# Optimization experiments

Measured on AMD Instinct MI355X. Metric: run time of the kernel, lower is better.

## Reference

```python
import jax, jax.numpy as jnp
from jax import lax
import numpy as np

B = 2048
NUM_COMPO = 650
NUM_CHARS = 27533
COMPO_SCORE_THRESH = 0.7
SCORE_ADJ_SCALE = 0.1
K = 10  # top-k chars and max padded hit indices


def setup_inputs() -> dict:
    key = jax.random.key(0)
    k1, k2, k3, k4, k5 = jax.random.split(key, 5)
    return {
        "pred_class_logits": jax.random.normal(k1, (B, NUM_CHARS), dtype=jnp.float32),
        "pred_compo_logits": jax.random.normal(k2, (B, NUM_COMPO), dtype=jnp.float32),
        "chinese_char_ids": jax.random.randint(k3, (B,), 0, NUM_CHARS, dtype=jnp.int32),
        "compo_co_occurrence_prob": jax.random.uniform(k4, (NUM_COMPO, NUM_COMPO), dtype=jnp.float32),
        "compo_chinese_matrix": jax.random.randint(k5, (NUM_COMPO, NUM_CHARS), 0, 2, dtype=jnp.int32),
    }


def _components_to_char(compo_scores, co_occ, matrix):
    """Per-sample: compo_scores [C], co_occ [C,C], matrix [C,V] (0/1 int)."""
    # score adjustment: sum over compos with score>0.88 of co_occ row * score * scale
    hi = compo_scores > 0.88
    w = jnp.where(hi, compo_scores, 0.0)                       # [C]
    adjusted = compo_scores + SCORE_ADJ_SCALE * (w @ co_occ)   # [C]
    max_idx = jnp.argmax(adjusted)
    max_score = compo_scores[max_idx]

    # select compos above threshold, sorted descending by score
    sel = compo_scores > COMPO_SCORE_THRESH
    num_sel = jnp.sum(sel.astype(jnp.int32))
    masked = jnp.where(sel, compo_scores, -jnp.inf)
    order = jnp.argsort(-masked)                                # selected first, desc
    sorted_scores = jnp.take(compo_scores, order)               # [C]

    hit0 = matrix[max_idx]                                      # [V] int

    def cond(st):
        i, hit, _prev = st
        return (i < num_sel) & (jnp.sum(hit) > 1)

    def body(st):
        i, hit, _prev = st
        comp = matrix[order[i]]
        new_hit = ((hit + comp) == 2).astype(hit.dtype)         # intersection
        return (i + 1, new_hit, hit)

    i, hit, prev = lax.while_loop(cond, body, (jnp.int32(1), hit0, hit0))
    num_hit = jnp.sum(hit)
    empty = num_hit == 0
    i = jnp.where(empty, i - 1, i)
    hit = jnp.where(empty, prev, hit)
    hit_score = jnp.where(i == 1, max_score, sorted_scores[i - 1])

    # first K indices where hit == 1, padded with -1 (fixed shape)
    ar = jnp.arange(NUM_CHARS, dtype=jnp.int32)
    vals = jnp.where(hit == 1, NUM_CHARS - ar, 0)
    topv, topi = lax.top_k(vals, K)
    hit_indices = jnp.where(topv > 0, topi.astype(jnp.int32), -1)
    return adjusted, hit_indices, hit_score


def reference(pred_class_logits, pred_compo_logits, chinese_char_ids,
              compo_co_occurrence_prob, compo_chinese_matrix):
    class_probs = jax.nn.softmax(pred_class_logits, axis=1)     # [B, V]
    compo_scores = jax.nn.sigmoid(pred_compo_logits)            # [B, C]
    class_scores, class_indices = lax.top_k(class_probs, K)     # [B, K]

    adjusted, hit_idx, hit_scores = jax.vmap(
        _components_to_char, in_axes=(0, None, None)
    )(compo_scores, compo_co_occurrence_prob, compo_chinese_matrix)

    num_hit = jnp.sum((hit_idx != -1).astype(jnp.int32), axis=1)  # [B]
    pred1 = jnp.where(num_hit == 1, hit_idx[:, 0], class_indices[:, 0])
    pred2 = jnp.where((class_scores[:, 0] < 0.85) & (num_hit == 1),
                      hit_idx[:, 0], class_indices[:, 0])

    hit_compare = jnp.any(class_indices[:, :, None] == hit_idx[:, None, :], axis=2)  # [B,K]
    j = jnp.argmax(hit_compare, axis=1)  # first True (all-False -> 0), matches stable desc argsort[0]
    pred3 = class_indices[jnp.arange(class_indices.shape[0]), j]

    return (class_indices, class_scores, compo_scores, adjusted,
            hit_idx, hit_scores, pred1, pred2, pred3)
```

## Files before the change

kernel.cpp:

```cpp
#include <hip/hip_runtime.h>
#include <math.h>

#define NB 2048
#define NC 650
#define NV 27533
#define NK 10
#define NWRD 861
#define NT 256
#define NCHUNK 11
#define CHPR 431

__global__ __launch_bounds__(NT) void pack_kernel(const int* __restrict__ mat,
                                                  unsigned* __restrict__ packed) {
  const int lane = threadIdx.x & 63;
  const int wave = (blockIdx.x * NT + threadIdx.x) >> 6;
  const int nw = (gridDim.x * NT) >> 6;
  for (int t = wave; t < NC * CHPR; t += nw) {
    int c = t / CHPR;
    int ch = t - c * CHPR;
    int e = (ch << 6) + lane;
    int val = (e < NV) ? mat[(size_t)c * NV + e] : 0;
    unsigned long long m = __ballot(val != 0);
    if (lane == 0) {
      size_t base = (size_t)c * NWRD + (ch << 1);
      packed[base] = (unsigned)m;
      if ((ch << 1) + 1 < NWRD) packed[base + 1] = (unsigned)(m >> 32);
    }
  }
}

__device__ __forceinline__ int block_sum(int v, volatile int* red4, int tid) {
#pragma unroll
  for (int off = 32; off > 0; off >>= 1) v += __shfl_down(v, off);
  if ((tid & 63) == 0) red4[tid >> 6] = v;
  __syncthreads();
  int tot = red4[0] + red4[1] + red4[2] + red4[3];
  __syncthreads();
  return tot;
}

__global__ __launch_bounds__(NT, 6) void gen_pred_kernel(
    const float* __restrict__ class_logits,
    const float* __restrict__ compo_logits,
    const float* __restrict__ co_occ,
    const unsigned* __restrict__ packed,
    float* __restrict__ out) {
  const int b = blockIdx.x;
  const int tid = threadIdx.x;
  const int lane = tid & 63;
  const int wid = tid >> 6;

  __shared__ __align__(16) char arena[10464];
  float* mv = (float*)arena;
  int* mi = (int*)(arena + 5120);
  float* s_score = (float*)arena;
  int* s_selidx = (int*)(arena + 2608);
  int* s_hi = (int*)(arena + 5216);
  int* s_order = (int*)(arena + 7824);

  __shared__ float red_f[4];
  __shared__ int red_i[4];
  __shared__ int s_cls_idx[NK];
  __shared__ float s_cls_sc[NK];
  __shared__ int s_hit[NK];
  __shared__ int s_hicnt[NCHUNK];
  __shared__ int s_selcnt[NCHUNK];

  const size_t o_cidx = 0;
  const size_t o_csc = (size_t)NB * NK;
  const size_t o_comp = 2 * (size_t)NB * NK;
  const size_t o_adj = o_comp + (size_t)NB * NC;
  const size_t o_hidx = o_adj + (size_t)NB * NC;
  const size_t o_hsc = o_hidx + (size_t)NB * NK;
  const size_t o_p1 = o_hsc + NB;
  const size_t o_p2 = o_p1 + NB;
  const size_t o_p3 = o_p2 + NB;

  const float* lg = class_logits + (size_t)b * NV;
  float tv[NK];
  int ti[NK];
#pragma unroll
  for (int k = 0; k < NK; k++) { tv[k] = -INFINITY; ti[k] = 0x7fffffff; }
  float ssum = 0.f;

#define PROC(val, idxv)                                                   \
  {                                                                       \
    float v_ = (val);                                                     \
    ssum += __expf(v_);                                                   \
    if (v_ > tv[NK - 1]) {                                                \
      tv[NK - 1] = v_; ti[NK - 1] = (idxv);                               \
      _Pragma("unroll")                                                   \
      for (int p_ = NK - 1; p_ > 0; p_--) {                               \
        if (tv[p_] > tv[p_ - 1]) {                                        \
          float t0_ = tv[p_]; tv[p_] = tv[p_ - 1]; tv[p_ - 1] = t0_;      \
          int t1_ = ti[p_]; ti[p_] = ti[p_ - 1]; ti[p_ - 1] = t1_;        \
        }                                                                 \
      }                                                                   \
    }                                                                     \
  }

  const int s0 = (4 - (b & 3)) & 3;
  const int M4 = (NV - s0) >> 2;
  if (tid < s0) PROC(lg[tid], tid);
  {
    const float4* lg4 = (const float4*)(lg + s0);
    int v = tid;
    float4 f;
    if (v < M4) f = lg4[v];
    while (v < M4) {
      int vn = v + NT;
      float4 fn = f;
      if (vn < M4) fn = lg4[vn];
      int base = s0 + (v << 2);
      PROC(f.x, base);
      PROC(f.y, base + 1);
      PROC(f.z, base + 2);
      PROC(f.w, base + 3);
      f = fn;
      v = vn;
    }
  }
  {
    int baseT = s0 + (M4 << 2);
    if (tid < NV - baseT) PROC(lg[baseT + tid], baseT + tid);
  }
#undef PROC

  {
    float s = ssum;
#pragma unroll
    for (int off = 32; off > 0; off >>= 1) s += __shfl_down(s, off);
    if (lane == 0) red_f[wid] = s;
  }
  __syncthreads();
  const float Sv = red_f[0] + red_f[1] + red_f[2] + red_f[3];
  __syncthreads();

  if (tid >= 128) {
#pragma unroll
    for (int k = 0; k < NK; k++) {
      mv[(tid - 128) * NK + k] = tv[k];
      mi[(tid - 128) * NK + k] = ti[k];
    }
  }
  __syncthreads();
  if (tid < 128) {
    float rv[NK]; int ri[NK];
    int pa = 0, pb = 0;
    int bb = tid * NK;
#pragma unroll
    for (int k = 0; k < NK; k++) {
      float va = tv[pa]; int ia = ti[pa];
      float vb = mv[bb + pb]; int ib = mi[bb + pb];
      bool ta = (va > vb) || (va == vb && ia < ib);
      if (ta) { rv[k] = va; ri[k] = ia; pa++; }
      else { rv[k] = vb; ri[k] = ib; pb++; }
    }
#pragma unroll
    for (int k = 0; k < NK; k++) { mv[bb + k] = rv[k]; mi[bb + k] = ri[k]; }
  }
  __syncthreads();
  for (int st = 64; st > 0; st >>= 1) {
    if (tid < st) {
      float rv[NK]; int ri[NK];
      int pa = 0, pb = 0;
      int ba = tid * NK, bb = (tid + st) * NK;
#pragma unroll
      for (int k = 0; k < NK; k++) {
        float va = mv[ba + pa]; int ia = mi[ba + pa];
        float vb = mv[bb + pb]; int ib = mi[bb + pb];
        bool ta = (va > vb) || (va == vb && ia < ib);
        if (ta) { rv[k] = va; ri[k] = ia; pa++; }
        else { rv[k] = vb; ri[k] = ib; pb++; }
      }
#pragma unroll
      for (int k = 0; k < NK; k++) { mv[ba + k] = rv[k]; mi[ba + k] = ri[k]; }
    }
    __syncthreads();
  }
  if (tid < NK) {
    int cidx = mi[tid];
    float sc = __expf(mv[tid]) / Sv;
    s_cls_idx[tid] = cidx;
    s_cls_sc[tid] = sc;
    out[o_cidx + (size_t)b * NK + tid] = (float)cidx;
    out[o_csc + (size_t)b * NK + tid] = sc;
  }
  __syncthreads();

  const float* cl = compo_logits + (size_t)b * NC;
  for (int j = tid; j < NC; j += NT) {
    float x = cl[j];
    float sc = 1.f / (1.f + expf(-x));
    s_score[j] = sc;
    out[o_comp + (size_t)b * NC + j] = sc;
  }
  __syncthreads();

  for (int c = wid; c < NCHUNK; c += 4) {
    int e = (c << 6) + lane;
    float s = (e < NC) ? s_score[e] : 0.f;
    unsigned long long mh = __ballot(s > 0.88f);
    unsigned long long ms = __ballot(s > 0.7f);
    if (lane == 0) { s_hicnt[c] = __popcll(mh); s_selcnt[c] = __popcll(ms); }
  }
  __syncthreads();
  int nhi = 0, nsel = 0;
#pragma unroll
  for (int q = 0; q < NCHUNK; q++) { nhi += s_hicnt[q]; nsel += s_selcnt[q]; }
  for (int c = wid; c < NCHUNK; c += 4) {
    int e = (c << 6) + lane;
    float s = (e < NC) ? s_score[e] : 0.f;
    unsigned long long mh = __ballot(s > 0.88f);
    unsigned long long ms = __ballot(s > 0.7f);
    int oh = 0, os = 0;
    for (int q = 0; q < c; q++) { oh += s_hicnt[q]; os += s_selcnt[q]; }
    unsigned long long lower = (1ull << lane) - 1ull;
    if (s > 0.88f) s_hi[oh + __popcll(mh & lower)] = e;
    if (s > 0.7f) s_selidx[os + __popcll(ms & lower)] = e;
  }
  __syncthreads();

  for (int t = tid; t < nsel; t += NT) {
    int j = s_selidx[t];
    float sj = s_score[j];
    int r = 0;
    for (int q = 0; q < nsel; q++) {
      int jq = s_selidx[q];
      float sq = s_score[jq];
      r += (sq > sj || (sq == sj && jq < j)) ? 1 : 0;
    }
    s_order[r] = j;
  }

  float bestv = -INFINITY;
  int besti = 0x7fffffff;
  for (int j = tid; j < NC; j += NT) {
    float acc = 0.f;
    for (int h = 0; h < nhi; h++) {
      int i2 = s_hi[h];
      acc = fmaf(s_score[i2], co_occ[(size_t)i2 * NC + j], acc);
    }
    float adj = s_score[j] + 0.1f * acc;
    out[o_adj + (size_t)b * NC + j] = adj;
    if (adj > bestv || (adj == bestv && j < besti)) { bestv = adj; besti = j; }
  }
#pragma unroll
  for (int off = 32; off > 0; off >>= 1) {
    float ov = __shfl_down(bestv, off);
    int oi = __shfl_down(besti, off);
    if (ov > bestv || (ov == bestv && oi < besti)) { bestv = ov; besti = oi; }
  }
  if (lane == 0) { red_f[wid] = bestv; red_i[wid] = besti; }
  __syncthreads();
  int max_idx;
  {
    float bv = red_f[0]; int bi = red_i[0];
#pragma unroll
    for (int q = 1; q < 4; q++) {
      float qv = red_f[q]; int qi = red_i[q];
      if (qv > bv || (qv == bv && qi < bi)) { bv = qv; bi = qi; }
    }
    max_idx = bi;
  }
  const float max_score = s_score[max_idx];
  __syncthreads();

  unsigned hw[4], pv[4], pf[4];
  int cnt, cnt_prev, i;
  {
    const unsigned* prow = packed + (size_t)max_idx * NWRD;
    int pc = 0;
#pragma unroll
    for (int t = 0; t < 4; t++) {
      int w = (tid << 2) + t;
      unsigned x = (w < NWRD) ? prow[w] : 0u;
      hw[t] = x;
      pv[t] = x;
      pc += __popc(x);
    }
    if (1 < nsel) {
      const unsigned* row = packed + (size_t)s_order[1] * NWRD;
#pragma unroll
      for (int t = 0; t < 4; t++) {
        int w = (tid << 2) + t;
        pf[t] = (w < NWRD) ? row[w] : 0u;
      }
    }
    cnt = block_sum(pc, red_i, tid);
    cnt_prev = cnt;
    i = 1;
    while (i < nsel && cnt > 1) {
      unsigned nx[4];
      int p2 = 0;
#pragma unroll
      for (int t = 0; t < 4; t++) {
        unsigned x = hw[t] & pf[t];
        nx[t] = x;
        p2 += __popc(x);
      }
      int inext = i + 1;
      if (inext < nsel) {
        const unsigned* row = packed + (size_t)s_order[inext] * NWRD;
#pragma unroll
        for (int t = 0; t < 4; t++) {
          int w = (tid << 2) + t;
          pf[t] = (w < NWRD) ? row[w] : 0u;
        }
      }
      int nc2 = block_sum(p2, red_i, tid);
#pragma unroll
      for (int t = 0; t < 4; t++) { pv[t] = hw[t]; hw[t] = nx[t]; }
      cnt_prev = cnt;
      cnt = nc2;
      i = inext;
    }
    if (cnt == 0 && i > 1) {
      i--;
      cnt = cnt_prev;
#pragma unroll
      for (int t = 0; t < 4; t++) hw[t] = pv[t];
    }
  }

  if (tid < NK) s_hit[tid] = -1;
  {
    int myc = 0;
#pragma unroll
    for (int t = 0; t < 4; t++) myc += __popc(hw[t]);
    int inc = myc;
#pragma unroll
    for (int off = 1; off < 64; off <<= 1) {
      int y = __shfl_up(inc, off);
      if (lane >= off) inc += y;
    }
    if (lane == 63) red_i[wid] = inc;
    __syncthreads();
    int excl = inc - myc;
    for (int q = 0; q < wid; q++) excl += red_i[q];
    int r = excl;
    if (r < NK) {
#pragma unroll
      for (int t = 0; t < 4; t++) {
        unsigned x = hw[t];
        int wb = ((tid << 2) + t) << 5;
        while (x && r < NK) {
          int bpos = __ffs(x) - 1;
          x &= x - 1;
          s_hit[r] = wb + bpos;
          r++;
        }
        if (r >= NK) break;
      }
    }
  }
  __syncthreads();

  int num_hit = cnt < NK ? cnt : NK;
  if (tid < NK) out[o_hidx + (size_t)b * NK + tid] = (float)s_hit[tid];
  if (tid == 0) {
    float hsc = (i <= 1) ? max_score : s_score[s_order[i - 1]];
    out[o_hsc + b] = hsc;
    int ci0 = s_cls_idx[0];
    float cs0 = s_cls_sc[0];
    int h0 = s_hit[0];
    int p1 = (num_hit == 1) ? h0 : ci0;
    int p2 = (cs0 < 0.85f && num_hit == 1) ? h0 : ci0;
    int jj = 0;
    for (int k = 0; k < NK; k++) {
      bool m = false;
#pragma unroll
      for (int q = 0; q < NK; q++) m = m || (s_cls_idx[k] == s_hit[q]);
      if (m) { jj = k; break; }
    }
    out[o_p1 + b] = (float)p1;
    out[o_p2 + b] = (float)p2;
    out[o_p3 + b] = (float)s_cls_idx[jj];
  }
}

extern "C" void kernel_launch(void* const* d_in, const int* in_sizes, int n_in,
                              void* d_out, int out_size, void* d_ws, size_t ws_size,
                              hipStream_t stream) {
  const float* class_logits = (const float*)d_in[0];
  const float* compo_logits = (const float*)d_in[1];
  const float* co_occ = (const float*)d_in[3];
  const int* mat = (const int*)d_in[4];
  float* out = (float*)d_out;
  unsigned* packed = (unsigned*)d_ws;

  pack_kernel<<<1280, NT, 0, stream>>>(mat, packed);
  gen_pred_kernel<<<NB, NT, 0, stream>>>(class_logits, compo_logits, co_occ,
                                         packed, out);
}
```

Baseline: 473.7 us.

## Replace per-thread top-k insertion with threshold-filtered two-pass top-k selection

```diff
diff --git a/kernel.cpp b/kernel.cpp
--- a/kernel.cpp
+++ b/kernel.cpp
@@ -9,23 +9,39 @@
 #define NT 256
 #define NCHUNK 11
 #define CHPR 431
+#define SVCAP 768
 
 __global__ __launch_bounds__(NT) void pack_kernel(const int* __restrict__ mat,
                                                   unsigned* __restrict__ packed) {
+  const int c = blockIdx.x >> 1;
+  const int half = blockIdx.x & 1;
   const int lane = threadIdx.x & 63;
-  const int wave = (blockIdx.x * NT + threadIdx.x) >> 6;
-  const int nw = (gridDim.x * NT) >> 6;
-  for (int t = wave; t < NC * CHPR; t += nw) {
-    int c = t / CHPR;
-    int ch = t - c * CHPR;
+  const int w4 = threadIdx.x >> 6;
+  const int ch0 = half ? 216 : 0;
+  const int ch1 = half ? CHPR : 216;
+  const int* row = mat + (size_t)c * NV;
+  const size_t obase = (size_t)c * NWRD;
+
+  int ch = ch0 + w4;
+  int val = 0;
+  if (ch < ch1) {
     int e = (ch << 6) + lane;
-    int val = (e < NV) ? mat[(size_t)c * NV + e] : 0;
+    val = (e < NV) ? row[e] : 0;
+  }
+  while (ch < ch1) {
+    int chn = ch + 4;
+    int valn = 0;
+    if (chn < ch1) {
+      int en = (chn << 6) + lane;
+      valn = (en < NV) ? row[en] : 0;
+    }
     unsigned long long m = __ballot(val != 0);
-    if (lane == 0) {
-      size_t base = (size_t)c * NWRD + (ch << 1);
-      packed[base] = (unsigned)m;
-      if ((ch << 1) + 1 < NWRD) packed[base + 1] = (unsigned)(m >> 32);
-    }
+    if (lane < 2) {
+      int wi = (ch << 1) + lane;
+      if (wi < NWRD) packed[obase + wi] = (unsigned)(m >> (lane * 32));
+    }
+    val = valn;
+    ch = chn;
   }
 }
 
@@ -39,7 +55,7 @@
   return tot;
 }
 
-__global__ __launch_bounds__(NT, 6) void gen_pred_kernel(
+__global__ __launch_bounds__(NT, 8) void gen_pred_kernel(
     const float* __restrict__ class_logits,
     const float* __restrict__ compo_logits,
     const float* __restrict__ co_occ,
@@ -51,15 +67,17 @@
   const int wid = tid >> 6;
 
   __shared__ __align__(16) char arena[10464];
-  float* mv = (float*)arena;
-  int* mi = (int*)(arena + 5120);
+  float* s_sv_v = (float*)arena;
+  int* s_sv_i = (int*)(arena + 3072);
   float* s_score = (float*)arena;
   int* s_selidx = (int*)(arena + 2608);
   int* s_hi = (int*)(arena + 5216);
   int* s_order = (int*)(arena + 7824);
 
   __shared__ float red_f[4];
+  __shared__ float red_s[4];
   __shared__ int red_i[4];
+  __shared__ int s_svcnt;
   __shared__ int s_cls_idx[NK];
   __shared__ float s_cls_sc[NK];
   __shared__ int s_hit[NK];
@@ -77,33 +95,15 @@
   const size_t o_p3 = o_p2 + NB;
 
   const float* lg = class_logits + (size_t)b * NV;
-  float tv[NK];
-  int ti[NK];
-#pragma unroll
-  for (int k = 0; k < NK; k++) { tv[k] = -INFINITY; ti[k] = 0x7fffffff; }
-  float ssum = 0.f;
-
-#define PROC(val, idxv)                                                   \
-  {                                                                       \
-    float v_ = (val);                                                     \
-    ssum += __expf(v_);                                                   \
-    if (v_ > tv[NK - 1]) {                                                \
-      tv[NK - 1] = v_; ti[NK - 1] = (idxv);                               \
-      _Pragma("unroll")                                                   \
-      for (int p_ = NK - 1; p_ > 0; p_--) {                               \
-        if (tv[p_] > tv[p_ - 1]) {                                        \
-          float t0_ = tv[p_]; tv[p_] = tv[p_ - 1]; tv[p_ - 1] = t0_;      \
-          int t1_ = ti[p_]; ti[p_] = ti[p_ - 1]; ti[p_ - 1] = t1_;        \
-        }                                                                 \
-      }                                                                   \
-    }                                                                     \
-  }
-
   const int s0 = (4 - (b & 3)) & 3;
   const int M4 = (NV - s0) >> 2;
-  if (tid < s0) PROC(lg[tid], tid);
-  {
-    const float4* lg4 = (const float4*)(lg + s0);
+  const int baseT = s0 + (M4 << 2);
+  const float4* lg4 = (const float4*)(lg + s0);
+
+  float mx = -INFINITY;
+  float ss0 = 0.f, ss1 = 0.f;
+  if (tid < s0) { float x = lg[tid]; ss0 += __expf(x); mx = fmaxf(mx, x); }
+  {
     int v = tid;
     float4 f;
     if (v < M4) f = lg4[v];
@@ -111,82 +111,104 @@
       int vn = v + NT;
       float4 fn = f;
       if (vn < M4) fn = lg4[vn];
-      int base = s0 + (v << 2);
-      PROC(f.x, base);
-      PROC(f.y, base + 1);
-      PROC(f.z, base + 2);
-      PROC(f.w, base + 3);
-      f = fn;
-      v = vn;
-    }
-  }
-  {
-    int baseT = s0 + (M4 << 2);
-    if (tid < NV - baseT) PROC(lg[baseT + tid], baseT + tid);
-  }
-#undef PROC
-
-  {
-    float s = ssum;
+      ss0 += __expf(f.x); ss1 += __expf(f.y);
+      ss0 += __expf(f.z); ss1 += __expf(f.w);
+      mx = fmaxf(mx, fmaxf(fmaxf(f.x, f.y), fmaxf(f.z, f.w)));
+      f = fn; v = vn;
+    }
+  }
+  if (tid < NV - baseT) { float x = lg[baseT + tid]; ss0 += __expf(x); mx = fmaxf(mx, x); }
+
+  {
+    float s = ss0 + ss1;
 #pragma unroll
     for (int off = 32; off > 0; off >>= 1) s += __shfl_down(s, off);
-    if (lane == 0) red_f[wid] = s;
-  }
-  __syncthreads();
-  const float Sv = red_f[0] + red_f[1] + red_f[2] + red_f[3];
-  __syncthreads();
-
-  if (tid >= 128) {
-#pragma unroll
-    for (int k = 0; k < NK; k++) {
-      mv[(tid - 128) * NK + k] = tv[k];
-      mi[(tid - 128) * NK + k] = ti[k];
-    }
-  }
-  __syncthreads();
-  if (tid < 128) {
-    float rv[NK]; int ri[NK];
-    int pa = 0, pb = 0;
-    int bb = tid * NK;
-#pragma unroll
-    for (int k = 0; k < NK; k++) {
-      float va = tv[pa]; int ia = ti[pa];
-      float vb = mv[bb + pb]; int ib = mi[bb + pb];
-      bool ta = (va > vb) || (va == vb && ia < ib);
-      if (ta) { rv[k] = va; ri[k] = ia; pa++; }
-      else { rv[k] = vb; ri[k] = ib; pb++; }
-    }
-#pragma unroll
-    for (int k = 0; k < NK; k++) { mv[bb + k] = rv[k]; mi[bb + k] = ri[k]; }
-  }
-  __syncthreads();
-  for (int st = 64; st > 0; st >>= 1) {
-    if (tid < st) {
-      float rv[NK]; int ri[NK];
-      int pa = 0, pb = 0;
-      int ba = tid * NK, bb = (tid + st) * NK;
-#pragma unroll
-      for (int k = 0; k < NK; k++) {
-        float va = mv[ba + pa]; int ia = mi[ba + pa];
-        float vb = mv[bb + pb]; int ib = mi[bb + pb];
-        bool ta = (va > vb) || (va == vb && ia < ib);
-        if (ta) { rv[k] = va; ri[k] = ia; pa++; }
-        else { rv[k] = vb; ri[k] = ib; pb++; }
-      }
-#pragma unroll
-      for (int k = 0; k < NK; k++) { mv[ba + k] = rv[k]; mi[ba + k] = ri[k]; }
-    }
-    __syncthreads();
-  }
+    float g = mx;
+    g = fmaxf(g, __shfl_xor(g, 1));
+    g = fmaxf(g, __shfl_xor(g, 2));
+    g = fmaxf(g, __shfl_xor(g, 4));
+    g = fmaxf(g, __shfl_xor(g, 8));
+    float t = fminf(g, __shfl_xor(g, 16));
+    t = fminf(t, __shfl_xor(t, 32));
+    if (lane == 0) { red_s[wid] = s; red_f[wid] = t; }
+  }
+  if (tid == 0) s_svcnt = 0;
+  __syncthreads();
+  const float Sv = red_s[0] + red_s[1] + red_s[2] + red_s[3];
+  const float T = fminf(fminf(red_f[0], red_f[1]), fminf(red_f[2], red_f[3]));
+
+#define SV_APPEND(pred, val, idxv)                                          \
+  {                                                                         \
+    bool p_ = (pred);                                                       \
+    unsigned long long m_ = __ballot(p_);                                   \
+    if (m_) {                                                               \
+      int leader_ = (int)(__ffsll(m_) - 1);                                 \
+      int base_ = 0;                                                        \
+      if (lane == leader_) base_ = atomicAdd(&s_svcnt, (int)__popcll(m_));  \
+      base_ = __shfl(base_, leader_);                                       \
+      if (p_) {                                                             \
+        int pos_ = base_ + (int)__popcll(m_ & ((1ull << lane) - 1ull));     \
+        if (pos_ < SVCAP) { s_sv_v[pos_] = (val); s_sv_i[pos_] = (idxv); }  \
+      }                                                                     \
+    }                                                                       \
+  }
+
+  if (wid == 0) {
+    bool p = (tid < s0) && (lg[tid] >= T);
+    float v = (tid < s0) ? lg[tid] : 0.f;
+    SV_APPEND(p, v, tid);
+  }
+  {
+    int v = tid;
+    float4 f;
+    if (v < M4) f = lg4[v];
+    while (v < M4) {
+      int vn = v + NT;
+      float4 fn = f;
+      if (vn < M4) fn = lg4[vn];
+      float m4 = fmaxf(fmaxf(f.x, f.y), fmaxf(f.z, f.w));
+      if (__ballot(m4 >= T)) {
+        int base = s0 + (v << 2);
+        SV_APPEND(f.x >= T, f.x, base);
+        SV_APPEND(f.y >= T, f.y, base + 1);
+        SV_APPEND(f.z >= T, f.z, base + 2);
+        SV_APPEND(f.w >= T, f.w, base + 3);
+      }
+      f = fn; v = vn;
+    }
+  }
+  if (wid == 0) {
+    int rem = NV - baseT;
+    bool p = (tid < rem) && (lg[baseT + tid] >= T);
+    float v = (tid < rem) ? lg[baseT + tid] : 0.f;
+    SV_APPEND(p, v, baseT + tid);
+  }
+#undef SV_APPEND
+  __syncthreads();
+
+  {
+    int S = s_svcnt;
+    if (S > SVCAP) S = SVCAP;
+    for (int t2 = tid; t2 < S; t2 += NT) {
+      float vt = s_sv_v[t2];
+      int it = s_sv_i[t2];
+      int r = 0;
+      for (int q = 0; q < S; q++) {
+        float vq = s_sv_v[q];
+        int iq = s_sv_i[q];
+        r += (vq > vt || (vq == vt && iq < it)) ? 1 : 0;
+      }
+      if (r < NK) { s_cls_idx[r] = it; s_cls_sc[r] = vt; }
+    }
+  }
+  __syncthreads();
   if (tid < NK) {
-    int cidx = mi[tid];
-    float sc = __expf(mv[tid]) / Sv;
-    s_cls_idx[tid] = cidx;
+    int cidx = s_cls_idx[tid];
+    float sc = __expf(s_cls_sc[tid]) / Sv;
     s_cls_sc[tid] = sc;
     out[o_cidx + (size_t)b * NK + tid] = (float)cidx;
     out[o_csc + (size_t)b * NK + tid] = sc;
   }
-  __syncthreads();
 
   const float* cl = compo_logits + (size_t)b * NC;
   for (int j = tid; j < NC; j += NT) {
@@ -389,7 +411,7 @@
   float* out = (float*)d_out;
   unsigned* packed = (unsigned*)d_ws;
 
-  pack_kernel<<<1280, NT, 0, stream>>>(mat, packed);
+  pack_kernel<<<2 * NC, NT, 0, stream>>>(mat, packed);
   gen_pred_kernel<<<NB, NT, 0, stream>>>(class_logits, compo_logits, co_occ,
                                          packed, out);
 }
```

Result: faster. 460.1 us (-2.9%).
